# Performance work log

Measured on AMD Instinct MI355X. Metric: run time of the kernel, lower is better.

Reference implementation:

```python
import jax, jax.numpy as jnp
import numpy as np

D_MODEL = 256
D_INNER = 512
D_STATE = 16
DT_RANK = 16
D_CONV = 4


def _layernorm(x, g, b):
    m = x.mean(-1, keepdims=True)
    v = jnp.mean((x - m) ** 2, axis=-1, keepdims=True)
    return (x - m) * jax.lax.rsqrt(v + 1e-5) * g + b


def _mamba(x, p):
    # x: (B, L, D); faithful to mamba_ssm Mamba forward (selective_scan_ref)
    in_w, conv_w, conv_b, xp_w, dt_w, dt_b, A_log, Dp, out_w = p
    B, L, _ = x.shape
    xz = x @ in_w.T                                   # (B, L, 2*d_inner)
    xi, z = jnp.split(xz, 2, axis=-1)
    # causal depthwise conv over time (d_conv=4), truncated to L
    xpad = jnp.pad(xi, ((0, 0), (D_CONV - 1, 0), (0, 0)))
    xc = conv_b + sum(xpad[:, k:k + L, :] * conv_w[:, k] for k in range(D_CONV))
    xc = jax.nn.silu(xc)                              # u: (B, L, d_inner)
    dbl = xc @ xp_w.T                                 # (B, L, dt_rank + 2*d_state)
    dt = dbl[..., :DT_RANK]
    Bm = dbl[..., DT_RANK:DT_RANK + D_STATE]          # (B, L, n)
    Cm = dbl[..., DT_RANK + D_STATE:]                 # (B, L, n)
    delta = jax.nn.softplus(dt @ dt_w.T + dt_b)       # (B, L, d_inner)
    A = -jnp.exp(A_log)                               # (d_inner, n)
    dA = jnp.exp(jnp.einsum('bld,dn->bldn', delta, A))
    dBu = jnp.einsum('bld,bln,bld->bldn', delta, Bm, xc)

    def step(h, inp):
        dA_t, dBu_t, C_t = inp
        h = dA_t * h + dBu_t                          # (B, d_inner, n)
        return h, jnp.einsum('bdn,bn->bd', h, C_t)

    h0 = jnp.zeros((B, D_INNER, D_STATE), x.dtype)
    _, ys = jax.lax.scan(step, h0, (dA.transpose(1, 0, 2, 3),
                                    dBu.transpose(1, 0, 2, 3),
                                    Cm.transpose(1, 0, 2)))
    y = ys.transpose(1, 0, 2) + xc * Dp               # (B, L, d_inner)
    y = y * jax.nn.silu(z)
    return y @ out_w.T                                # (B, L, D)


def _encoder(layer_params, x):
    # layer_params leaves have leading axis = num_layers (3)
    def step(carry, p):
        h = _layernorm(carry, p[0], p[1])
        return h + _mamba(h, p[2:]), None
    out, _ = jax.lax.scan(step, x, layer_params)
    return out


def _forward(x1, x2, x3, x4, audio, vis_w, vis_b, ln_g, ln_b, in_w, conv_w,
             conv_b, xp_w, dt_w, dt_b, A_log, Dp, out_w, gate_w, gate_b):
    gamma = 1.0
    bt = x1.shape[0]
    B = bt // 10
    d = x1.shape[1]
    pooled = [x.mean((2, 3)).reshape(B, 10, d) for x in (x1, x2, x3, x4)]
    vis = [p @ vis_w[i].T + vis_b[i] for i, p in enumerate(pooled)]
    # encoders 0..3: audio, 4..7: video scales
    stacked = jnp.stack([audio, audio, audio, audio] + vis)     # (8, B, 10, d)
    enc_params = (ln_g, ln_b, in_w, conv_w, conv_b, xp_w, dt_w, dt_b, A_log, Dp, out_w)
    outs = jax.vmap(_encoder)(enc_params, stacked)              # (8, B, 10, d)
    gates = jax.nn.silu(jnp.einsum('ebld,eod->eblo', outs, gate_w)
                        + gate_b[:, None, None, :])
    # NOTE: gate1 is reshaped WITHOUT transpose (faithful to original code)
    ag1 = gates[0].reshape(bt, d, 1, 1)
    ag2 = jnp.transpose(gates[1], (1, 0, 2)).reshape(bt, d, 1, 1)
    ag3 = jnp.transpose(gates[2], (1, 0, 2)).reshape(bt, d, 1, 1)
    ag4 = jnp.transpose(gates[3], (1, 0, 2)).reshape(bt, d, 1, 1)
    vg = sum(jnp.transpose(gates[4 + i], (1, 0, 2)).reshape(bt, d)
             for i in range(4)) / 4.0
    x1o = x1 + ag1 * x1 * gamma
    x2o = x2 + ag2 * x2 * gamma
    x3o = x3 + ag3 * x3 * gamma
    x4o = x4 + ag4 * x4 * gamma
    af = audio.reshape(bt, d)
    ao = (af + vg * af * gamma)[:, :, None]                     # (bt, d, 1)
    return (x4o, x3o, x2o, x1o, ao)


def setup_inputs() -> dict:
    key = jax.random.key(0)
    ks = jax.random.split(key, 24)
    s = 0.05
    n = lambda k, shp: jax.random.normal(k, shp, dtype=jnp.float32)
    inp = {
        'x1': n(ks[0], (40, 256, 56, 56)),
        'x2': n(ks[1], (40, 256, 28, 28)),
        'x3': n(ks[2], (40, 256, 14, 14)),
        'x4': n(ks[3], (40, 256, 7, 7)),
        'audio': n(ks[4], (4, 10, 256)),
        'vis_w': n(ks[5], (4, 256, 256)) * s,
        'vis_b': n(ks[6], (4, 256)) * s,
        'ln_g': jnp.ones((8, 3, 256), jnp.float32),
        'ln_b': jnp.zeros((8, 3, 256), jnp.float32),
        'in_w': n(ks[7], (8, 3, 1024, 256)) * s,
        'conv_w': n(ks[8], (8, 3, 512, 4)) * s,
        'conv_b': n(ks[9], (8, 3, 512)) * s,
        'xp_w': n(ks[10], (8, 3, 48, 512)) * s,
        'dt_w': n(ks[11], (8, 3, 512, 16)) * s,
        'dt_b': n(ks[12], (8, 3, 512)) * s,
        'A_log': jnp.broadcast_to(jnp.log(jnp.arange(1, 17, dtype=jnp.float32)),
                                  (8, 3, 512, 16)) + 0.0,
        'Dp': jnp.ones((8, 3, 512), jnp.float32),
        'out_w': n(ks[13], (8, 3, 256, 512)) * s,
        'gate_w': n(ks[14], (8, 256, 256)) * s,
        'gate_b': n(ks[15], (8, 256)) * s,
    }
    return inp


def reference(x1, x2, x3, x4, audio, vis_w, vis_b, ln_g, ln_b, in_w, conv_w,
              conv_b, xp_w, dt_w, dt_b, A_log, Dp, out_w, gate_w, gate_b):
    return _forward(x1, x2, x3, x4, audio, vis_w, vis_b, ln_g, ln_b, in_w,
                    conv_w, conv_b, xp_w, dt_w, dt_b, A_log, Dp, out_w,
                    gate_w, gate_b)
```

## Files before the change

kernel.cpp:

```cpp
#include <hip/hip_runtime.h>

#define DM 256
#define DI 512
#define NL 10

#define WS_POOLED 0
#define WS_GATES  40960
#define WS_SX     122880
#define WS_SH     204800
#define WS_XC     286720
#define WS_SZ     450560
#define WS_Y2     614400
#define WS_DBL    778240

__device__ __forceinline__ float dot4(float4 a, float4 b) {
    return a.x*b.x + a.y*b.y + a.z*b.z + a.w*b.w;
}
__device__ __forceinline__ float silu(float x) {
    return x / (1.f + __expf(-x));
}

__global__ void pool_kernel(const float* __restrict__ x1, const float* __restrict__ x2,
                            const float* __restrict__ x3, const float* __restrict__ x4,
                            const float* __restrict__ audio, float* __restrict__ ws)
{
    if (blockIdx.x >= 10240) {
        const int idx = blockIdx.x - 10240, e = idx >> 2, b = idx & 3;
        float* sx = ws + WS_SX + (e*4+b)*2560;
        for (int i = threadIdx.x; i < 2560; i += 256) sx[i] = audio[b*2560 + i];
        return;
    }
    float* pooled = ws + WS_POOLED;
    int wid  = (blockIdx.x * blockDim.x + threadIdx.x) >> 6;
    int lane = threadIdx.x & 63;
    int img = wid / 10240;
    int r   = wid % 10240;
    const float* src; int hw;
    if      (img == 0) { src = x1; hw = 3136; }
    else if (img == 1) { src = x2; hw = 784; }
    else if (img == 2) { src = x3; hw = 196; }
    else               { src = x4; hw = 49; }
    const float* row = src + (size_t)r * hw;
    float s = 0.f;
    if (hw == 49) {
        if (lane < 49) s = row[lane];
    } else {
        int n4 = hw >> 2;
        for (int j = lane; j < n4; j += 64) {
            float4 v = *(const float4*)(row + j*4);
            s += v.x + v.y + v.z + v.w;
        }
    }
    #pragma unroll
    for (int off = 32; off; off >>= 1) s += __shfl_down(s, off);
    if (lane == 0) pooled[img*10240 + r] = s / (float)hw;
}

__global__ __launch_bounds__(256)
void build_kernel(const float* __restrict__ vis_w, const float* __restrict__ vis_b,
                  float* __restrict__ ws)
{
    __shared__ float act[NL*DM];
    const int tid = threadIdx.x, bi = blockIdx.x;
    const int img = bi >> 6, b = (bi >> 4) & 3, tile = bi & 15;
    const float* pooled = ws + WS_POOLED + img*10240 + b*2560;
    for (int i = tid; i < 640; i += 256)
        ((float4*)act)[i] = ((const float4*)pooled)[i];
    __syncthreads();
    const int wave = tid >> 6, lane = tid & 63;
    const int c4 = lane >> 4, k16 = lane & 15;
    const int col = tile*16 + wave*4 + c4;
    const float* wp = vis_w + img*65536 + col*256 + k16*4;
    float acc[NL];
    #pragma unroll
    for (int l = 0; l < NL; l++) acc[l] = 0.f;
    #pragma unroll
    for (int ko = 0; ko < 4; ko++) {
        float4 wv = *(const float4*)(wp + ko*64);
        #pragma unroll
        for (int l = 0; l < NL; l++)
            acc[l] += dot4(wv, *(const float4*)(&act[l*256 + ko*64 + k16*4]));
    }
    #pragma unroll
    for (int l = 0; l < NL; l++) {
        acc[l] += __shfl_xor(acc[l], 1);
        acc[l] += __shfl_xor(acc[l], 2);
        acc[l] += __shfl_xor(acc[l], 4);
        acc[l] += __shfl_xor(acc[l], 8);
    }
    if (k16 == 0) {
        float bias = vis_b[img*256 + col];
        float* sx = ws + WS_SX + ((img+4)*4+b)*2560;
        #pragma unroll
        for (int l = 0; l < NL; l++) sx[l*256 + col] = bias + acc[l];
    }
}

__global__ __launch_bounds__(256)
void lnxz_kernel(const float* __restrict__ ln_g, const float* __restrict__ ln_b,
                 const float* __restrict__ in_w, const float* __restrict__ conv_w,
                 const float* __restrict__ conv_b, float* __restrict__ ws, int layer)
{
    __shared__ float act[NL*DM];
    const int tid = threadIdx.x, bi = blockIdx.x;
    const int e = bi >> 8, b = (bi >> 6) & 3, tile = bi & 63;
    const int el = e*3 + layer;
    const int wave = tid >> 6, lane = tid & 63;
    const float* sx = ws + WS_SX + (e*4+b)*2560;
    float* shg = ws + WS_SH + (e*4+b)*2560;

    for (int l = wave; l < NL; l += 4) {
        float4 v = *(const float4*)(sx + l*256 + lane*4);
        float s = v.x+v.y+v.z+v.w, ss = dot4(v, v);
        #pragma unroll
        for (int off = 32; off; off >>= 1) { s += __shfl_xor(s, off); ss += __shfl_xor(ss, off); }
        float m = s * (1.f/256.f);
        float rs = rsqrtf(ss*(1.f/256.f) - m*m + 1e-5f);
        float4 gv = *(const float4*)(ln_g + el*256 + lane*4);
        float4 bv = *(const float4*)(ln_b + el*256 + lane*4);
        float4 hv;
        hv.x = (v.x-m)*rs*gv.x + bv.x;
        hv.y = (v.y-m)*rs*gv.y + bv.y;
        hv.z = (v.z-m)*rs*gv.z + bv.z;
        hv.w = (v.w-m)*rs*gv.w + bv.w;
        *(float4*)(&act[l*256 + lane*4]) = hv;
        if (tile == 0) *(float4*)(shg + l*256 + lane*4) = hv;
    }
    __syncthreads();

    const int c4 = lane >> 4, k16 = lane & 15;
    const int col = tile*16 + wave*4 + c4;
    const float* wp = in_w + (size_t)el*262144 + (size_t)col*256 + k16*4;
    float acc[NL];
    #pragma unroll
    for (int l = 0; l < NL; l++) acc[l] = 0.f;
    #pragma unroll
    for (int ko = 0; ko < 4; ko++) {
        float4 wv = *(const float4*)(wp + ko*64);
        #pragma unroll
        for (int l = 0; l < NL; l++)
            acc[l] += dot4(wv, *(const float4*)(&act[l*256 + ko*64 + k16*4]));
    }
    #pragma unroll
    for (int l = 0; l < NL; l++) {
        acc[l] += __shfl_xor(acc[l], 1);
        acc[l] += __shfl_xor(acc[l], 2);
        acc[l] += __shfl_xor(acc[l], 4);
        acc[l] += __shfl_xor(acc[l], 8);
    }
    if (k16 == 0) {
        if (col < 512) {
            float4 cw = *(const float4*)(conv_w + el*2048 + col*4);
            float cb = conv_b[el*512 + col];
            float* xc = ws + WS_XC + (e*4+b)*5120;
            float x0 = 0.f, x1 = 0.f, x2 = 0.f;
            #pragma unroll
            for (int l = 0; l < NL; l++) {
                float x3 = acc[l];
                float a = cb + x3*cw.w + x2*cw.z + x1*cw.y + x0*cw.x;
                xc[l*512 + col] = silu(a);
                x0 = x1; x1 = x2; x2 = x3;
            }
        } else {
            float* sz = ws + WS_SZ + (e*4+b)*5120;
            const int d = col - 512;
            #pragma unroll
            for (int l = 0; l < NL; l++) sz[l*512 + d] = silu(acc[l]);
        }
    }
}

__global__ __launch_bounds__(256)
void dbl_kernel(const float* __restrict__ xp_w, float* __restrict__ ws, int layer)
{
    __shared__ float xc_l[NL*DI];
    const int tid = threadIdx.x, bi = blockIdx.x;
    const int e = bi >> 5, b = (bi >> 3) & 3, s = bi & 7;
    const int el = e*3 + layer;
    const float* xc = ws + WS_XC + (e*4+b)*5120;
    for (int i = tid; i < 1280; i += 256)
        ((float4*)xc_l)[i] = ((const float4*)xc)[i];
    __syncthreads();

    const int wave = tid >> 6, lane = tid & 63;
    const int c4 = lane >> 4, k16 = lane & 15;
    float* dbl = ws + WS_DBL + (e*4+b)*480;
    #pragma unroll
    for (int i = 0; i < 4; i++) {
        int t = wave*16 + i*4 + c4;
        if (t < 60) {
            int l = t / 6, r = s*6 + t % 6;
            const float* wp = xp_w + el*24576 + r*512 + k16*4;
            float p = 0.f;
            #pragma unroll
            for (int ko = 0; ko < 8; ko++)
                p += dot4(*(const float4*)(wp + ko*64),
                          *(const float4*)(&xc_l[l*512 + ko*64 + k16*4]));
            p += __shfl_xor(p, 1);
            p += __shfl_xor(p, 2);
            p += __shfl_xor(p, 4);
            p += __shfl_xor(p, 8);
            if (k16 == 0) dbl[l*48 + r] = p;
        }
    }
}

__global__ __launch_bounds__(128)
void scan_kernel(const float* __restrict__ dt_w, const float* __restrict__ dt_b,
                 const float* __restrict__ A_log, const float* __restrict__ Dp,
                 float* __restrict__ ws, int layer)
{
    __shared__ float dbl_l[NL*48];
    const int tid = threadIdx.x, bi = blockIdx.x;
    const int e = bi >> 4, b = (bi >> 2) & 3, ch = bi & 3;
    const int el = e*3 + layer;
    const int eb = e*4 + b;
    for (int i = tid; i < 480; i += 128) dbl_l[i] = ws[WS_DBL + eb*480 + i];
    __syncthreads();

    const int d = ch*128 + tid;
    const float* dwp = dt_w + el*8192 + d*16;
    float4 dw0 = *(const float4*)(dwp);
    float4 dw1 = *(const float4*)(dwp + 4);
    float4 dw2 = *(const float4*)(dwp + 8);
    float4 dw3 = *(const float4*)(dwp + 12);
    float dbv = dt_b[el*512 + d];
    float Dpv = Dp[el*512 + d];
    float Av[16];
    #pragma unroll
    for (int n = 0; n < 16; n++) Av[n] = -__expf(A_log[el*8192 + d*16 + n]);
    const float* xc = ws + WS_XC + eb*5120;
    const float* sz = ws + WS_SZ + eb*5120;
    float* y2 = ws + WS_Y2 + eb*5120;
    float h[16];
    #pragma unroll
    for (int n = 0; n < 16; n++) h[n] = 0.f;
    #pragma unroll
    for (int l = 0; l < NL; l++) {
        float4 t0 = *(const float4*)(&dbl_l[l*48]);
        float4 t1 = *(const float4*)(&dbl_l[l*48 + 4]);
        float4 t2 = *(const float4*)(&dbl_l[l*48 + 8]);
        float4 t3 = *(const float4*)(&dbl_l[l*48 + 12]);
        float a = dbv + dot4(t0,dw0) + dot4(t1,dw1) + dot4(t2,dw2) + dot4(t3,dw3);
        float dl = fmaxf(a, 0.f) + log1pf(__expf(-fabsf(a)));
        float xcv = xc[l*512 + d];
        float du = dl * xcv;
        float y = 0.f;
        #pragma unroll
        for (int n = 0; n < 16; n++) {
            float Bn = dbl_l[l*48 + 16 + n];
            float Cn = dbl_l[l*48 + 32 + n];
            h[n] = __expf(dl*Av[n])*h[n] + du*Bn;
            y += h[n]*Cn;
        }
        y2[l*512 + d] = (y + xcv*Dpv) * sz[l*512 + d];
    }
}

__global__ __launch_bounds__(256)
void out_kernel(const float* __restrict__ out_w, float* __restrict__ ws, int layer)
{
    __shared__ float act[NL*DI];
    const int tid = threadIdx.x, bi = blockIdx.x;
    const int e = bi >> 6, b = (bi >> 4) & 3, tile = bi & 15;
    const int el = e*3 + layer;
    const float* y2 = ws + WS_Y2 + (e*4+b)*5120;
    for (int i = tid; i < 1280; i += 256)
        ((float4*)act)[i] = ((const float4*)y2)[i];
    __syncthreads();

    const int wave = tid >> 6, lane = tid & 63;
    const int c4 = lane >> 4, k16 = lane & 15;
    const int col = tile*16 + wave*4 + c4;
    const float* wp = out_w + (size_t)el*131072 + (size_t)col*512 + k16*4;
    float acc[NL];
    #pragma unroll
    for (int l = 0; l < NL; l++) acc[l] = 0.f;
    #pragma unroll
    for (int ko = 0; ko < 8; ko++) {
        float4 wv = *(const float4*)(wp + ko*64);
        #pragma unroll
        for (int l = 0; l < NL; l++)
            acc[l] += dot4(wv, *(const float4*)(&act[l*512 + ko*64 + k16*4]));
    }
    #pragma unroll
    for (int l = 0; l < NL; l++) {
        acc[l] += __shfl_xor(acc[l], 1);
        acc[l] += __shfl_xor(acc[l], 2);
        acc[l] += __shfl_xor(acc[l], 4);
        acc[l] += __shfl_xor(acc[l], 8);
    }
    if (k16 == 0) {
        const float* sh = ws + WS_SH + (e*4+b)*2560;
        float* sx = ws + WS_SX + (e*4+b)*2560;
        #pragma unroll
        for (int l = 0; l < NL; l++) sx[l*256 + col] = sh[l*256 + col] + acc[l];
    }
}

__global__ __launch_bounds__(256)
void gate_kernel(const float* __restrict__ gate_w, const float* __restrict__ gate_b,
                 float* __restrict__ ws)
{
    __shared__ float act[NL*DM];
    const int tid = threadIdx.x, bi = blockIdx.x;
    const int e = bi >> 6, b = (bi >> 4) & 3, tile = bi & 15;
    const float* sx = ws + WS_SX + (e*4+b)*2560;
    for (int i = tid; i < 640; i += 256)
        ((float4*)act)[i] = ((const float4*)sx)[i];
    __syncthreads();

    const int wave = tid >> 6, lane = tid & 63;
    const int c4 = lane >> 4, k16 = lane & 15;
    const int col = tile*16 + wave*4 + c4;
    const float* wp = gate_w + e*65536 + col*256 + k16*4;
    float acc[NL];
    #pragma unroll
    for (int l = 0; l < NL; l++) acc[l] = 0.f;
    #pragma unroll
    for (int ko = 0; ko < 4; ko++) {
        float4 wv = *(const float4*)(wp + ko*64);
        #pragma unroll
        for (int l = 0; l < NL; l++)
            acc[l] += dot4(wv, *(const float4*)(&act[l*256 + ko*64 + k16*4]));
    }
    #pragma unroll
    for (int l = 0; l < NL; l++) {
        acc[l] += __shfl_xor(acc[l], 1);
        acc[l] += __shfl_xor(acc[l], 2);
        acc[l] += __shfl_xor(acc[l], 4);
        acc[l] += __shfl_xor(acc[l], 8);
    }
    if (k16 == 0) {
        float gb = gate_b[e*256 + col];
        float* gates = ws + WS_GATES;
        #pragma unroll
        for (int l = 0; l < NL; l++)
            gates[(e*40 + b*10 + l)*256 + col] = silu(gb + acc[l]);
    }
}

__global__ void scale_ao_kernel(const float* __restrict__ x1, const float* __restrict__ x2,
                                const float* __restrict__ x3, const float* __restrict__ x4,
                                const float* __restrict__ audio,
                                const float* __restrict__ gates, float* __restrict__ out)
{
    int wid  = (blockIdx.x * blockDim.x + threadIdx.x) >> 6;
    int lane = threadIdx.x & 63;
    if (wid >= 41120) return;
    if (wid >= 40960) {
        int i = (wid - 40960)*64 + lane;
        int bt = i >> 8, c = i & 255;
        int lb = (bt & 3)*10 + (bt >> 2);
        float vg = 0.25f * (gates[(160 + lb)*256 + c] + gates[(200 + lb)*256 + c] +
                            gates[(240 + lb)*256 + c] + gates[(280 + lb)*256 + c]);
        out[42649600 + i] = audio[i] * (1.f + vg);
        return;
    }
    int t = wid / 10240, r = wid % 10240;
    int bt = r >> 8, c = r & 255;
    int lb = (bt & 3)*10 + (bt >> 2);
    const float* src; int hw; size_t obase; int gidx;
    if      (t == 0) { src = x4; hw = 49;   obase = 0;        gidx = (120 + lb)*256 + c; }
    else if (t == 1) { src = x3; hw = 196;  obase = 501760;   gidx = ( 80 + lb)*256 + c; }
    else if (t == 2) { src = x2; hw = 784;  obase = 2508800;  gidx = ( 40 + lb)*256 + c; }
    else             { src = x1; hw = 3136; obase = 10536960; gidx = r; }
    float scale = 1.f + gates[gidx];
    const float* row = src + (size_t)r * hw;
    float* orow = out + obase + (size_t)r * hw;
    if (hw == 49) {
        if (lane < 49) orow[lane] = row[lane] * scale;
    } else {
        int n4 = hw >> 2;
        for (int j = lane; j < n4; j += 64) {
            float4 v = *(const float4*)(row + j*4);
            v.x *= scale; v.y *= scale; v.z *= scale; v.w *= scale;
            *(float4*)(orow + j*4) = v;
        }
    }
}

extern "C" void kernel_launch(void* const* d_in, const int* in_sizes, int n_in,
                              void* d_out, int out_size, void* d_ws, size_t ws_size,
                              hipStream_t stream)
{
    const float* x1     = (const float*)d_in[0];
    const float* x2     = (const float*)d_in[1];
    const float* x3     = (const float*)d_in[2];
    const float* x4     = (const float*)d_in[3];
    const float* audio  = (const float*)d_in[4];
    const float* vis_w  = (const float*)d_in[5];
    const float* vis_b  = (const float*)d_in[6];
    const float* ln_g   = (const float*)d_in[7];
    const float* ln_b   = (const float*)d_in[8];
    const float* in_w   = (const float*)d_in[9];
    const float* conv_w = (const float*)d_in[10];
    const float* conv_b = (const float*)d_in[11];
    const float* xp_w   = (const float*)d_in[12];
    const float* dt_w   = (const float*)d_in[13];
    const float* dt_b   = (const float*)d_in[14];
    const float* A_log  = (const float*)d_in[15];
    const float* Dp     = (const float*)d_in[16];
    const float* out_w  = (const float*)d_in[17];
    const float* gate_w = (const float*)d_in[18];
    const float* gate_b = (const float*)d_in[19];

    float* ws  = (float*)d_ws;
    float* out = (float*)d_out;

    pool_kernel<<<dim3(10256), dim3(256), 0, stream>>>(x1, x2, x3, x4, audio, ws);
    build_kernel<<<dim3(256), dim3(256), 0, stream>>>(vis_w, vis_b, ws);
    for (int layer = 0; layer < 3; layer++) {
        lnxz_kernel<<<dim3(2048), dim3(256), 0, stream>>>(ln_g, ln_b, in_w, conv_w,
                                                          conv_b, ws, layer);
        dbl_kernel<<<dim3(256), dim3(256), 0, stream>>>(xp_w, ws, layer);
        scan_kernel<<<dim3(128), dim3(128), 0, stream>>>(dt_w, dt_b, A_log, Dp, ws, layer);
        out_kernel<<<dim3(512), dim3(256), 0, stream>>>(out_w, ws, layer);
    }
    gate_kernel<<<dim3(512), dim3(256), 0, stream>>>(gate_w, gate_b, ws);
    scale_ao_kernel<<<dim3(10280), dim3(256), 0, stream>>>(x1, x2, x3, x4, audio,
                                                           ws + WS_GATES, out);
}
```

Measured before the change: 218.8 us.

## Fuse x_proj, selective scan and out_proj into one kernel per layer

Merges the dbl, scan and out kernels into a single dso_kernel. Each of the 512 blocks recomputes the full x_proj projection and the full scan for its (expert, batch) pair in shared memory, then computes its own 16-column tile of out_proj. This removes two kernel launches per layer and the global round-trips for dbl and y2. The cost is that the x_proj and scan work is repeated 16 times, once per output tile.

Result: slower. 358.0 us (+63.7%).

```diff
diff --git a/kernel.cpp b/kernel.cpp
--- a/kernel.cpp
+++ b/kernel.cpp
@@ -10,8 +10,6 @@
 #define WS_SH     204800
 #define WS_XC     286720
 #define WS_SZ     450560
-#define WS_Y2     614400
-#define WS_DBL    778240
 
 __device__ __forceinline__ float dot4(float4 a, float4 b) {
     return a.x*b.x + a.y*b.y + a.z*b.z + a.w*b.w;
@@ -171,106 +169,83 @@
 }
 
 __global__ __launch_bounds__(256)
-void dbl_kernel(const float* __restrict__ xp_w, float* __restrict__ ws, int layer)
+void dso_kernel(const float* __restrict__ xp_w, const float* __restrict__ dt_w,
+                const float* __restrict__ dt_b, const float* __restrict__ A_log,
+                const float* __restrict__ Dp,   const float* __restrict__ out_w,
+                float* __restrict__ ws, int layer)
 {
     __shared__ float xc_l[NL*DI];
-    const int tid = threadIdx.x, bi = blockIdx.x;
-    const int e = bi >> 5, b = (bi >> 3) & 3, s = bi & 7;
-    const int el = e*3 + layer;
-    const float* xc = ws + WS_XC + (e*4+b)*5120;
-    for (int i = tid; i < 1280; i += 256)
-        ((float4*)xc_l)[i] = ((const float4*)xc)[i];
-    __syncthreads();
-
-    const int wave = tid >> 6, lane = tid & 63;
-    const int c4 = lane >> 4, k16 = lane & 15;
-    float* dbl = ws + WS_DBL + (e*4+b)*480;
-    #pragma unroll
-    for (int i = 0; i < 4; i++) {
-        int t = wave*16 + i*4 + c4;
-        if (t < 60) {
-            int l = t / 6, r = s*6 + t % 6;
-            const float* wp = xp_w + el*24576 + r*512 + k16*4;
-            float p = 0.f;
-            #pragma unroll
-            for (int ko = 0; ko < 8; ko++)
-                p += dot4(*(const float4*)(wp + ko*64),
-                          *(const float4*)(&xc_l[l*512 + ko*64 + k16*4]));
-            p += __shfl_xor(p, 1);
-            p += __shfl_xor(p, 2);
-            p += __shfl_xor(p, 4);
-            p += __shfl_xor(p, 8);
-            if (k16 == 0) dbl[l*48 + r] = p;
-        }
-    }
-}
-
-__global__ __launch_bounds__(128)
-void scan_kernel(const float* __restrict__ dt_w, const float* __restrict__ dt_b,
-                 const float* __restrict__ A_log, const float* __restrict__ Dp,
-                 float* __restrict__ ws, int layer)
-{
+    __shared__ float y2_l[NL*DI];
     __shared__ float dbl_l[NL*48];
-    const int tid = threadIdx.x, bi = blockIdx.x;
-    const int e = bi >> 4, b = (bi >> 2) & 3, ch = bi & 3;
-    const int el = e*3 + layer;
-    const int eb = e*4 + b;
-    for (int i = tid; i < 480; i += 128) dbl_l[i] = ws[WS_DBL + eb*480 + i];
-    __syncthreads();
-
-    const int d = ch*128 + tid;
-    const float* dwp = dt_w + el*8192 + d*16;
-    float4 dw0 = *(const float4*)(dwp);
-    float4 dw1 = *(const float4*)(dwp + 4);
-    float4 dw2 = *(const float4*)(dwp + 8);
-    float4 dw3 = *(const float4*)(dwp + 12);
-    float dbv = dt_b[el*512 + d];
-    float Dpv = Dp[el*512 + d];
-    float Av[16];
-    #pragma unroll
-    for (int n = 0; n < 16; n++) Av[n] = -__expf(A_log[el*8192 + d*16 + n]);
-    const float* xc = ws + WS_XC + eb*5120;
-    const float* sz = ws + WS_SZ + eb*5120;
-    float* y2 = ws + WS_Y2 + eb*5120;
-    float h[16];
-    #pragma unroll
-    for (int n = 0; n < 16; n++) h[n] = 0.f;
-    #pragma unroll
-    for (int l = 0; l < NL; l++) {
-        float4 t0 = *(const float4*)(&dbl_l[l*48]);
-        float4 t1 = *(const float4*)(&dbl_l[l*48 + 4]);
-        float4 t2 = *(const float4*)(&dbl_l[l*48 + 8]);
-        float4 t3 = *(const float4*)(&dbl_l[l*48 + 12]);
-        float a = dbv + dot4(t0,dw0) + dot4(t1,dw1) + dot4(t2,dw2) + dot4(t3,dw3);
-        float dl = fmaxf(a, 0.f) + log1pf(__expf(-fabsf(a)));
-        float xcv = xc[l*512 + d];
-        float du = dl * xcv;
-        float y = 0.f;
-        #pragma unroll
-        for (int n = 0; n < 16; n++) {
-            float Bn = dbl_l[l*48 + 16 + n];
-            float Cn = dbl_l[l*48 + 32 + n];
-            h[n] = __expf(dl*Av[n])*h[n] + du*Bn;
-            y += h[n]*Cn;
-        }
-        y2[l*512 + d] = (y + xcv*Dpv) * sz[l*512 + d];
-    }
-}
-
-__global__ __launch_bounds__(256)
-void out_kernel(const float* __restrict__ out_w, float* __restrict__ ws, int layer)
-{
-    __shared__ float act[NL*DI];
     const int tid = threadIdx.x, bi = blockIdx.x;
     const int e = bi >> 6, b = (bi >> 4) & 3, tile = bi & 15;
     const int el = e*3 + layer;
-    const float* y2 = ws + WS_Y2 + (e*4+b)*5120;
+    const int eb = e*4 + b;
+    const float* xc = ws + WS_XC + eb*5120;
+    const float* sz = ws + WS_SZ + eb*5120;
+
     for (int i = tid; i < 1280; i += 256)
-        ((float4*)act)[i] = ((const float4*)y2)[i];
+        ((float4*)xc_l)[i] = ((const float4*)xc)[i];
     __syncthreads();
 
     const int wave = tid >> 6, lane = tid & 63;
     const int c4 = lane >> 4, k16 = lane & 15;
+
+    for (int i = 0; i < 30; i++) {
+        int t = wave*120 + i*4 + c4;
+        int l = t / 48, r = t % 48;
+        const float* wp = xp_w + el*24576 + r*512 + k16*4;
+        float p = 0.f;
+        #pragma unroll
+        for (int ko = 0; ko < 8; ko++)
+            p += dot4(*(const float4*)(wp + ko*64),
+                      *(const float4*)(&xc_l[l*512 + ko*64 + k16*4]));
+        p += __shfl_xor(p, 1);
+        p += __shfl_xor(p, 2);
+        p += __shfl_xor(p, 4);
+        p += __shfl_xor(p, 8);
+        if (k16 == 0) dbl_l[l*48 + r] = p;
+    }
+    __syncthreads();
+
+    for (int ch = 0; ch < 2; ch++) {
+        const int d = ch*256 + tid;
+        const float* dwp = dt_w + el*8192 + d*16;
+        float4 dw0 = *(const float4*)(dwp);
+        float4 dw1 = *(const float4*)(dwp + 4);
+        float4 dw2 = *(const float4*)(dwp + 8);
+        float4 dw3 = *(const float4*)(dwp + 12);
+        float dbv = dt_b[el*512 + d];
+        float Dpv = Dp[el*512 + d];
+        float Av[16];
+        #pragma unroll
+        for (int n = 0; n < 16; n++) Av[n] = -__expf(A_log[el*8192 + d*16 + n]);
+        float h[16];
+        #pragma unroll
+        for (int n = 0; n < 16; n++) h[n] = 0.f;
+        #pragma unroll
+        for (int l = 0; l < NL; l++) {
+            float4 t0 = *(const float4*)(&dbl_l[l*48]);
+            float4 t1 = *(const float4*)(&dbl_l[l*48 + 4]);
+            float4 t2 = *(const float4*)(&dbl_l[l*48 + 8]);
+            float4 t3 = *(const float4*)(&dbl_l[l*48 + 12]);
+            float a = dbv + dot4(t0,dw0) + dot4(t1,dw1) + dot4(t2,dw2) + dot4(t3,dw3);
+            float dl = fmaxf(a, 0.f) + log1pf(__expf(-fabsf(a)));
+            float xcv = xc_l[l*512 + d];
+            float du = dl * xcv;
+            float y = 0.f;
+            #pragma unroll
+            for (int n = 0; n < 16; n++) {
+                float Bn = dbl_l[l*48 + 16 + n];
+                float Cn = dbl_l[l*48 + 32 + n];
+                h[n] = __expf(dl*Av[n])*h[n] + du*Bn;
+                y += h[n]*Cn;
+            }
+            y2_l[l*512 + d] = (y + xcv*Dpv) * sz[l*512 + d];
+        }
+    }
+    __syncthreads();
+
     const int col = tile*16 + wave*4 + c4;
     const float* wp = out_w + (size_t)el*131072 + (size_t)col*512 + k16*4;
     float acc[NL];
@@ -281,7 +256,7 @@
         float4 wv = *(const float4*)(wp + ko*64);
         #pragma unroll
         for (int l = 0; l < NL; l++)
-            acc[l] += dot4(wv, *(const float4*)(&act[l*512 + ko*64 + k16*4]));
+            acc[l] += dot4(wv, *(const float4*)(&y2_l[l*512 + ko*64 + k16*4]));
     }
     #pragma unroll
     for (int l = 0; l < NL; l++) {
@@ -291,8 +266,8 @@
         acc[l] += __shfl_xor(acc[l], 8);
     }
     if (k16 == 0) {
-        const float* sh = ws + WS_SH + (e*4+b)*2560;
-        float* sx = ws + WS_SX + (e*4+b)*2560;
+        const float* sh = ws + WS_SH + eb*2560;
+        float* sx = ws + WS_SX + eb*2560;
         #pragma unroll
         for (int l = 0; l < NL; l++) sx[l*256 + col] = sh[l*256 + col] + acc[l];
     }
@@ -413,9 +388,8 @@
     for (int layer = 0; layer < 3; layer++) {
         lnxz_kernel<<<dim3(2048), dim3(256), 0, stream>>>(ln_g, ln_b, in_w, conv_w,
                                                           conv_b, ws, layer);
-        dbl_kernel<<<dim3(256), dim3(256), 0, stream>>>(xp_w, ws, layer);
-        scan_kernel<<<dim3(128), dim3(128), 0, stream>>>(dt_w, dt_b, A_log, Dp, ws, layer);
-        out_kernel<<<dim3(512), dim3(256), 0, stream>>>(out_w, ws, layer);
+        dso_kernel<<<dim3(512), dim3(256), 0, stream>>>(xp_w, dt_w, dt_b, A_log, Dp,
+                                                        out_w, ws, layer);
     }
     gate_kernel<<<dim3(512), dim3(256), 0, stream>>>(gate_w, gate_b, ws);
     scale_ao_kernel<<<dim3(10280), dim3(256), 0, stream>>>(x1, x2, x3, x4, audio,
```

## Fuse x_proj GEMV and selective scan into one kernel, split state across thread pairs

Applied to the files above, without the earlier changes.

Merges the dbl projection and the scan kernels into a single launch per layer. The 480-element dbl vector now stays in shared memory instead of taking a global round trip, and xc is read from shared memory. Each block recomputes the full dbl row for its (e,b), so the projection work is done four times over, once per channel chunk. The scan also splits the 16 states across two lanes with a shuffle reduction, which doubles thread-level parallelism. In exchange, there is redundant GEMV work and 128 blocks instead of 256 for the projection stage.

Measured after the change: 247.7 us. 13.3% more time.

```diff
diff --git a/kernel.cpp b/kernel.cpp
--- a/kernel.cpp
+++ b/kernel.cpp
@@ -11,7 +11,6 @@
 #define WS_XC     286720
 #define WS_SZ     450560
 #define WS_Y2     614400
-#define WS_DBL    778240
 
 __device__ __forceinline__ float dot4(float4 a, float4 b) {
     return a.x*b.x + a.y*b.y + a.z*b.z + a.w*b.w;
@@ -171,25 +170,27 @@
 }
 
 __global__ __launch_bounds__(256)
-void dbl_kernel(const float* __restrict__ xp_w, float* __restrict__ ws, int layer)
+void dblscan2_kernel(const float* __restrict__ xp_w, const float* __restrict__ dt_w,
+                     const float* __restrict__ dt_b, const float* __restrict__ A_log,
+                     const float* __restrict__ Dp,   float* __restrict__ ws, int layer)
 {
     __shared__ float xc_l[NL*DI];
+    __shared__ float dbl_l[NL*48];
     const int tid = threadIdx.x, bi = blockIdx.x;
-    const int e = bi >> 5, b = (bi >> 3) & 3, s = bi & 7;
-    const int el = e*3 + layer;
-    const float* xc = ws + WS_XC + (e*4+b)*5120;
+    const int e = bi >> 4, b = (bi >> 2) & 3, ch = bi & 3;
+    const int el = e*3 + layer, eb = e*4 + b;
+    const float* xc = ws + WS_XC + eb*5120;
+
     for (int i = tid; i < 1280; i += 256)
         ((float4*)xc_l)[i] = ((const float4*)xc)[i];
     __syncthreads();
 
-    const int wave = tid >> 6, lane = tid & 63;
-    const int c4 = lane >> 4, k16 = lane & 15;
-    float* dbl = ws + WS_DBL + (e*4+b)*480;
-    #pragma unroll
-    for (int i = 0; i < 4; i++) {
-        int t = wave*16 + i*4 + c4;
-        if (t < 60) {
-            int l = t / 6, r = s*6 + t % 6;
+    {
+        const int wave = tid >> 6, lane = tid & 63;
+        const int c4 = lane >> 4, k16 = lane & 15;
+        for (int i = 0; i < 30; i++) {
+            int t = wave*120 + i*4 + c4;
+            int l = t / 48, r = t % 48;
             const float* wp = xp_w + el*24576 + r*512 + k16*4;
             float p = 0.f;
             #pragma unroll
@@ -200,60 +201,51 @@
             p += __shfl_xor(p, 2);
             p += __shfl_xor(p, 4);
             p += __shfl_xor(p, 8);
-            if (k16 == 0) dbl[l*48 + r] = p;
+            if (k16 == 0) dbl_l[l*48 + r] = p;
         }
     }
-}
-
-__global__ __launch_bounds__(128)
-void scan_kernel(const float* __restrict__ dt_w, const float* __restrict__ dt_b,
-                 const float* __restrict__ A_log, const float* __restrict__ Dp,
-                 float* __restrict__ ws, int layer)
-{
-    __shared__ float dbl_l[NL*48];
-    const int tid = threadIdx.x, bi = blockIdx.x;
-    const int e = bi >> 4, b = (bi >> 2) & 3, ch = bi & 3;
-    const int el = e*3 + layer;
-    const int eb = e*4 + b;
-    for (int i = tid; i < 480; i += 128) dbl_l[i] = ws[WS_DBL + eb*480 + i];
-    __syncthreads();
-
-    const int d = ch*128 + tid;
-    const float* dwp = dt_w + el*8192 + d*16;
-    float4 dw0 = *(const float4*)(dwp);
-    float4 dw1 = *(const float4*)(dwp + 4);
-    float4 dw2 = *(const float4*)(dwp + 8);
-    float4 dw3 = *(const float4*)(dwp + 12);
-    float dbv = dt_b[el*512 + d];
-    float Dpv = Dp[el*512 + d];
-    float Av[16];
-    #pragma unroll
-    for (int n = 0; n < 16; n++) Av[n] = -__expf(A_log[el*8192 + d*16 + n]);
-    const float* xc = ws + WS_XC + eb*5120;
-    const float* sz = ws + WS_SZ + eb*5120;
-    float* y2 = ws + WS_Y2 + eb*5120;
-    float h[16];
-    #pragma unroll
-    for (int n = 0; n < 16; n++) h[n] = 0.f;
-    #pragma unroll
-    for (int l = 0; l < NL; l++) {
-        float4 t0 = *(const float4*)(&dbl_l[l*48]);
-        float4 t1 = *(const float4*)(&dbl_l[l*48 + 4]);
-        float4 t2 = *(const float4*)(&dbl_l[l*48 + 8]);
-        float4 t3 = *(const float4*)(&dbl_l[l*48 + 12]);
-        float a = dbv + dot4(t0,dw0) + dot4(t1,dw1) + dot4(t2,dw2) + dot4(t3,dw3);
-        float dl = fmaxf(a, 0.f) + log1pf(__expf(-fabsf(a)));
-        float xcv = xc[l*512 + d];
-        float du = dl * xcv;
-        float y = 0.f;
-        #pragma unroll
-        for (int n = 0; n < 16; n++) {
-            float Bn = dbl_l[l*48 + 16 + n];
-            float Cn = dbl_l[l*48 + 32 + n];
-            h[n] = __expf(dl*Av[n])*h[n] + du*Bn;
-            y += h[n]*Cn;
+    __syncthreads();
+
+    {
+        const int d = ch*128 + (tid >> 1);
+        const int half = tid & 1;
+        const float* dwp = dt_w + el*8192 + d*16;
+        float4 dw0 = *(const float4*)(dwp);
+        float4 dw1 = *(const float4*)(dwp + 4);
+        float4 dw2 = *(const float4*)(dwp + 8);
+        float4 dw3 = *(const float4*)(dwp + 12);
+        float dbv = dt_b[el*512 + d];
+        float Dpv = Dp[el*512 + d];
+        float Av[8];
+        #pragma unroll
+        for (int j = 0; j < 8; j++)
+            Av[j] = -__expf(A_log[el*8192 + d*16 + half*8 + j]);
+        const float* sz = ws + WS_SZ + eb*5120;
+        float* y2 = ws + WS_Y2 + eb*5120;
+        float h[8];
+        #pragma unroll
+        for (int j = 0; j < 8; j++) h[j] = 0.f;
+        #pragma unroll
+        for (int l = 0; l < NL; l++) {
+            float4 t0 = *(const float4*)(&dbl_l[l*48]);
+            float4 t1 = *(const float4*)(&dbl_l[l*48 + 4]);
+            float4 t2 = *(const float4*)(&dbl_l[l*48 + 8]);
+            float4 t3 = *(const float4*)(&dbl_l[l*48 + 12]);
+            float a = dbv + dot4(t0,dw0) + dot4(t1,dw1) + dot4(t2,dw2) + dot4(t3,dw3);
+            float dl = fmaxf(a, 0.f) + log1pf(__expf(-fabsf(a)));
+            float xcv = xc_l[l*512 + d];
+            float du = dl * xcv;
+            float y = 0.f;
+            #pragma unroll
+            for (int j = 0; j < 8; j++) {
+                float Bn = dbl_l[l*48 + 16 + half*8 + j];
+                float Cn = dbl_l[l*48 + 32 + half*8 + j];
+                h[j] = __expf(dl*Av[j])*h[j] + du*Bn;
+                y += h[j]*Cn;
+            }
+            y += __shfl_xor(y, 1);
+            if (!half) y2[l*512 + d] = (y + xcv*Dpv) * sz[l*512 + d];
         }
-        y2[l*512 + d] = (y + xcv*Dpv) * sz[l*512 + d];
     }
 }
 
@@ -413,8 +405,8 @@
     for (int layer = 0; layer < 3; layer++) {
         lnxz_kernel<<<dim3(2048), dim3(256), 0, stream>>>(ln_g, ln_b, in_w, conv_w,
                                                           conv_b, ws, layer);
-        dbl_kernel<<<dim3(256), dim3(256), 0, stream>>>(xp_w, ws, layer);
-        scan_kernel<<<dim3(128), dim3(128), 0, stream>>>(dt_w, dt_b, A_log, Dp, ws, layer);
+        dblscan2_kernel<<<dim3(128), dim3(256), 0, stream>>>(xp_w, dt_w, dt_b, A_log,
+                                                             Dp, ws, layer);
         out_kernel<<<dim3(512), dim3(256), 0, stream>>>(out_w, ws, layer);
     }
     gate_kernel<<<dim3(512), dim3(256), 0, stream>>>(gate_w, gate_b, ws);
```
